# Kernel optimization log

Measured on AMD Instinct MI355X. Metric: run time of the kernel, lower is better.

Reference implementation:

```python
import jax, jax.numpy as jnp
import numpy as np

N_NODES = 50000
NEG_SLOPE = 0.2  # PyG GATConv default leaky-relu slope


def _gat_conv(x, edge_index, W, a_src, a_dst, bias, heads, out_ch, concat, num_nodes):
    # x: [N, F_in]; W: [F_in, heads*out_ch]; a_src/a_dst: [heads, out_ch]; bias: [heads*out_ch] or [out_ch]
    h = (x @ W).reshape(num_nodes, heads, out_ch)            # [N,H,C]
    alpha_src = jnp.einsum('nhc,hc->nh', h, a_src)           # [N,H]
    alpha_dst = jnp.einsum('nhc,hc->nh', h, a_dst)           # [N,H]
    src, dst = edge_index[0], edge_index[1]
    e = jax.nn.leaky_relu(alpha_src[src] + alpha_dst[dst], NEG_SLOPE)  # [E,H]
    # segment softmax over incoming edges per destination (self-loops guarantee non-empty segments)
    m = jax.ops.segment_max(e, dst, num_segments=num_nodes)
    e = jnp.exp(e - m[dst])
    denom = jax.ops.segment_sum(e, dst, num_segments=num_nodes)
    alpha = e / denom[dst]                                    # [E,H]
    msg = h[src] * alpha[:, :, None]                          # [E,H,C]
    out = jax.ops.segment_sum(msg, dst, num_segments=num_nodes)  # [N,H,C]
    if concat:
        out = out.reshape(num_nodes, heads * out_ch)
    else:
        out = out.mean(axis=1)
    return out + bias


def _add_self_loops(edge_index, num_nodes):
    loops = jnp.arange(num_nodes, dtype=edge_index.dtype)
    return jnp.concatenate([edge_index, jnp.stack([loops, loops])], axis=1)


def setup_inputs() -> dict:
    key = jax.random.key(0)
    ks = jax.random.split(key, 16)
    N, F_in, H, C_hid, C_out = N_NODES, 128, 4, 64, 64
    E = 800000
    x = jax.random.normal(ks[0], (N, F_in), dtype=jnp.float32)
    edge_index = jax.random.randint(ks[1], (2, E), 0, N, dtype=jnp.int32)
    s = lambda fan: 1.0 / np.sqrt(fan)
    inp = {
        'x': x, 'edge_index': edge_index,
        'W1': jax.random.normal(ks[2], (F_in, H * C_hid), jnp.float32) * s(F_in),
        'a_src1': jax.random.normal(ks[3], (H, C_hid), jnp.float32) * s(C_hid),
        'a_dst1': jax.random.normal(ks[4], (H, C_hid), jnp.float32) * s(C_hid),
        'b1': jnp.zeros((H * C_hid,), jnp.float32),
        'W2': jax.random.normal(ks[5], (H * C_hid, H * C_hid), jnp.float32) * s(H * C_hid),
        'a_src2': jax.random.normal(ks[6], (H, C_hid), jnp.float32) * s(C_hid),
        'a_dst2': jax.random.normal(ks[7], (H, C_hid), jnp.float32) * s(C_hid),
        'b2': jnp.zeros((H * C_hid,), jnp.float32),
        'W3': jax.random.normal(ks[8], (H * C_hid, C_out), jnp.float32) * s(H * C_hid),
        'a_src3': jax.random.normal(ks[9], (1, C_out), jnp.float32) * s(C_out),
        'a_dst3': jax.random.normal(ks[10], (1, C_out), jnp.float32) * s(C_out),
        'b3': jnp.zeros((C_out,), jnp.float32),
    }
    return inp


def reference(x, edge_index, W1, a_src1, a_dst1, b1, W2, a_src2, a_dst2, b2, W3, a_src3, a_dst3, b3):
    N = x.shape[0]
    ei = _add_self_loops(edge_index, N)
    h = _gat_conv(x, ei, W1, a_src1, a_dst1, b1, heads=4, out_ch=64, concat=True, num_nodes=N)
    h = jax.nn.elu(h)
    h = _gat_conv(h, ei, W2, a_src2, a_dst2, b2, heads=4, out_ch=64, concat=True, num_nodes=N)
    h = jax.nn.elu(h)
    out = _gat_conv(h, ei, W3, a_src3, a_dst3, b3, heads=1, out_ch=64, concat=False, num_nodes=N)
    return out
```

## Files before the change

### kernel.cpp

```cpp
#include <hip/hip_runtime.h>
#include <hip/hip_fp16.h>
#include <cstdint>


typedef _Float16 f16;
typedef _Float16 f16x8 __attribute__((ext_vector_type(8)));
typedef float f32x4 __attribute__((ext_vector_type(4)));

__global__ __launch_bounds__(256) void count_kernel(const int* __restrict__ ei,
                                                    int E, int N,
                                                    int* __restrict__ deg) {
  int g = blockIdx.x * 256 + threadIdx.x;
  if (g >= E + N) return;
  int dst = (g < E) ? ei[E + g] : (g - E);
  atomicAdd(&deg[dst], 1);
}

__global__ __launch_bounds__(256) void deg_block_reduce(const int* __restrict__ deg,
                                                        int* __restrict__ bsum, int N) {
  __shared__ int red[4];
  int b = blockIdx.x;
  int v = 0;
#pragma unroll
  for (int s = 0; s < 4; ++s) {
    int idx = b * 1024 + s * 256 + threadIdx.x;
    if (idx < N) v += deg[idx];
  }
  for (int off = 32; off; off >>= 1) v += __shfl_down(v, off);
  if ((threadIdx.x & 63) == 0) red[threadIdx.x >> 6] = v;
  __syncthreads();
  if (threadIdx.x == 0) bsum[b] = red[0] + red[1] + red[2] + red[3];
}

__global__ __launch_bounds__(1024) void small_scan(const int* __restrict__ bsum,
                                                   int* __restrict__ bpre, int NB) {
  __shared__ int buf[1024];
  int v = (threadIdx.x < NB) ? bsum[threadIdx.x] : 0;
  buf[threadIdx.x] = v;
  __syncthreads();
  for (int off = 1; off < 1024; off <<= 1) {
    int tv = (threadIdx.x >= off) ? buf[threadIdx.x - off] : 0;
    __syncthreads();
    buf[threadIdx.x] += tv;
    __syncthreads();
  }
  if (threadIdx.x < NB) bpre[threadIdx.x] = buf[threadIdx.x] - v;
}

__global__ __launch_bounds__(1024) void scan_final(const int* __restrict__ deg,
                                                   const int* __restrict__ bpre,
                                                   int* __restrict__ row_off,
                                                   int* __restrict__ cursor,
                                                   int N, int total) {
  __shared__ int buf[1024];
  int b = blockIdx.x;
  int i = b * 1024 + threadIdx.x;
  int v = (i < N) ? deg[i] : 0;
  buf[threadIdx.x] = v;
  __syncthreads();
  for (int off = 1; off < 1024; off <<= 1) {
    int tv = (threadIdx.x >= off) ? buf[threadIdx.x - off] : 0;
    __syncthreads();
    buf[threadIdx.x] += tv;
    __syncthreads();
  }
  if (i < N) {
    int ro = bpre[b] + buf[threadIdx.x] - v;
    row_off[i] = ro;
    cursor[i] = ro;
  }
  if (i == 0) row_off[N] = total;
}

__global__ __launch_bounds__(256) void scatter_kernel(const int* __restrict__ ei,
                                                      int E, int N,
                                                      int* __restrict__ cursor,
                                                      int* __restrict__ esrc,
                                                      int* __restrict__ edst) {
  int g = blockIdx.x * 256 + threadIdx.x;
  if (g >= E + N) return;
  int src, dst;
  if (g < E) { src = ei[g]; dst = ei[E + g]; }
  else       { src = g - E; dst = src; }
  int pos = atomicAdd(&cursor[dst], 1);
  esrc[pos] = src;
  edst[pos] = dst;
}

__global__ __launch_bounds__(256) void convert_wt_all(
    const float* __restrict__ W1, const float* __restrict__ W2,
    const float* __restrict__ W3, f16* __restrict__ Wt1, f16* __restrict__ Wt2,
    f16* __restrict__ Wt3, int n1, int n2, int n3, int N1, int N2, int N3,
    int K1, int K2, int K3) {
  int t = blockIdx.x * 256 + threadIdx.x;
  if (t < n1) {
    int n = t % N1, k = t / N1;
    Wt1[(size_t)n * K1 + k] = (f16)W1[t];
    return;
  }
  t -= n1;
  if (t < n2) {
    int n = t % N2, k = t / N2;
    Wt2[(size_t)n * K2 + k] = (f16)W2[t];
    return;
  }
  t -= n2;
  if (t < n3) {
    int n = t % N3, k = t / N3;
    Wt3[(size_t)n * K3 + k] = (f16)W3[t];
  }
}

template <int BN, bool ACAST>
__global__ __launch_bounds__(256) void mfma_gemm_alpha(
    const void* __restrict__ Ap_, const f16* __restrict__ Bt,
    f16* __restrict__ Tout,
    const float* __restrict__ avec_src, const float* __restrict__ avec_dst,
    float* __restrict__ asrc, float* __restrict__ adst,
    int M, int K, int Ncol) {
  constexpr int RF = (BN == 128) ? 4 : 2;
  __shared__ f16 As[128][40];
  __shared__ f16 Bs[BN][40];
  int tid = threadIdx.x;
  int wv = tid >> 6, lane = tid & 63;
  int lrow = lane & 15, lkb = lane >> 4;
  int row0 = blockIdx.x * 128, col0 = blockIdx.y * BN;
  int wro = (BN == 128) ? (wv >> 1) * 64 : wv * 32;
  int wco = (BN == 128) ? (wv & 1) * 64 : 0;
  int hg = (col0 + wco) >> 6;

  f32x4 acc[RF][4];
#pragma unroll
  for (int rf = 0; rf < RF; ++rf)
#pragma unroll
    for (int cf = 0; cf < 4; ++cf) acc[rf][cf] = (f32x4){0.f, 0.f, 0.f, 0.f};

  for (int kk = 0; kk < K; kk += 32) {
#pragma unroll
    for (int q = 0; q < 2; ++q) {
      int slot = tid + q * 256;
      int r = slot >> 2, ko = (slot & 3) << 3;
      int gr = min(row0 + r, M - 1);
      if (ACAST) {
        const float* Af = (const float*)Ap_ + (size_t)gr * K + kk + ko;
        float4 v0 = *reinterpret_cast<const float4*>(Af);
        float4 v1 = *reinterpret_cast<const float4*>(Af + 4);
        f16 o[8] = {(f16)v0.x, (f16)v0.y, (f16)v0.z, (f16)v0.w,
                    (f16)v1.x, (f16)v1.y, (f16)v1.z, (f16)v1.w};
        *reinterpret_cast<f16x8*>(&As[r][ko]) = *reinterpret_cast<f16x8*>(o);
      } else {
        *reinterpret_cast<f16x8*>(&As[r][ko]) =
            *reinterpret_cast<const f16x8*>((const f16*)Ap_ + (size_t)gr * K + kk + ko);
      }
    }
#pragma unroll
    for (int q = 0; q < BN / 64; ++q) {
      int slot = tid + q * 256;
      int c = slot >> 2, ko = (slot & 3) << 3;
      *reinterpret_cast<f16x8*>(&Bs[c][ko]) =
          *reinterpret_cast<const f16x8*>(&Bt[(size_t)(col0 + c) * K + kk + ko]);
    }
    __syncthreads();
    f16x8 af[RF], bf[4];
#pragma unroll
    for (int rf = 0; rf < RF; ++rf)
      af[rf] = *reinterpret_cast<f16x8*>(&As[wro + rf * 16 + lrow][lkb * 8]);
#pragma unroll
    for (int cf = 0; cf < 4; ++cf)
      bf[cf] = *reinterpret_cast<f16x8*>(&Bs[wco + cf * 16 + lrow][lkb * 8]);
#pragma unroll
    for (int rf = 0; rf < RF; ++rf)
#pragma unroll
      for (int cf = 0; cf < 4; ++cf)
        acc[rf][cf] = __builtin_amdgcn_mfma_f32_16x16x32_f16(af[rf], bf[cf],
                                                             acc[rf][cf], 0, 0, 0);
    __syncthreads();
  }

  int Hh = Ncol >> 6;
  float avs[4], avd[4];
#pragma unroll
  for (int cf = 0; cf < 4; ++cf) {
    avs[cf] = avec_src[hg * 64 + cf * 16 + lrow];
    avd[cf] = avec_dst[hg * 64 + cf * 16 + lrow];
  }

#pragma unroll
  for (int rf = 0; rf < RF; ++rf) {
#pragma unroll
    for (int r = 0; r < 4; ++r) {
      float ps = 0.f, pd = 0.f;
#pragma unroll
      for (int cf = 0; cf < 4; ++cf) {
        float v = acc[rf][cf][r];
        ps = fmaf(v, avs[cf], ps);
        pd = fmaf(v, avd[cf], pd);
      }
#pragma unroll
      for (int off = 1; off < 16; off <<= 1) {
        ps += __shfl_xor(ps, off);
        pd += __shfl_xor(pd, off);
      }
      int row = row0 + wro + rf * 16 + lkb * 4 + r;
      if (lrow == 0 && row < M) {
        asrc[row * Hh + hg] = ps;
        adst[row * Hh + hg] = pd;
      }
    }
#pragma unroll
    for (int r = 0; r < 4; ++r) {
      int row = row0 + wro + rf * 16 + lkb * 4 + r;
      if (row < M) {
#pragma unroll
        for (int cf = 0; cf < 4; ++cf)
          Tout[(size_t)row * Ncol + col0 + wco + cf * 16 + lrow] =
              (f16)acc[rf][cf][r];
      }
    }
  }
}

__global__ __launch_bounds__(256) void edge_weights_h4(
    const int* __restrict__ esrc, const int* __restrict__ edst,
    const float* __restrict__ asrc, const float* __restrict__ adst,
    float* __restrict__ w, int ET) {
  int t = blockIdx.x * 256 + threadIdx.x;
  if (t >= ET * 4) return;
  int j = t >> 2, h = t & 3;
  float e = asrc[esrc[j] * 4 + h] + adst[edst[j] * 4 + h];
  e = fmaxf(e, 0.2f * e);
  w[t] = __expf(e);
}

__global__ __launch_bounds__(256) void edge_weights_h1(
    const int* __restrict__ esrc, const int* __restrict__ edst,
    const float* __restrict__ asrc, const float* __restrict__ adst,
    float* __restrict__ w, int ET) {
  int j = blockIdx.x * 256 + threadIdx.x;
  if (j >= ET) return;
  float e = asrc[esrc[j]] + adst[edst[j]];
  e = fmaxf(e, 0.2f * e);
  w[j] = __expf(e);
}

template <bool ELU>
__global__ __launch_bounds__(256) void aggregate_h4(
    const f16* __restrict__ T16, const int* __restrict__ row_off,
    const int* __restrict__ esrc, const float* __restrict__ w,
    const float* __restrict__ bias, f16* __restrict__ outF, int N) {
  int wv = threadIdx.x >> 6, lane = threadIdx.x & 63;
  int dst = blockIdx.x * 4 + wv;
  if (dst >= N) return;
  int head = lane >> 4;
  int hsel = lane & 48;
  int r0 = row_off[dst], r1 = row_off[dst + 1];
  const char* tbase = reinterpret_cast<const char*>(T16);
  uint loff = (uint)lane * 8;
  float den = 0.f, ax = 0.f, ay = 0.f, az = 0.f, aw = 0.f;
  for (int base = r0; base < r1; base += 8) {
    int jb = base + (lane & 7);
    int sv = 0;
    float wl = 0.f;
    if (jb < r1) {
      sv = esrc[jb];
      wl = w[(jb << 2) + head];
    }
#pragma unroll
    for (int i = 0; i < 8; ++i) {
      int sj = __shfl(sv, i);
      float wj = __shfl(wl, hsel + i);
      den += wj;
      uint2 raw = *reinterpret_cast<const uint2*>(tbase + (((uint)sj << 9) + loff));
      __half2 p0 = *reinterpret_cast<__half2*>(&raw.x);
      __half2 p1 = *reinterpret_cast<__half2*>(&raw.y);
      float2 f0 = __half22float2(p0);
      float2 f1 = __half22float2(p1);
      ax = fmaf(wj, f0.x, ax);
      ay = fmaf(wj, f0.y, ay);
      az = fmaf(wj, f1.x, az);
      aw = fmaf(wj, f1.y, aw);
    }
  }
  float rd = 1.f / den;
  float4 bv = *reinterpret_cast<const float4*>(&bias[lane << 2]);
  float vx = ax * rd + bv.x, vy = ay * rd + bv.y;
  float vz = az * rd + bv.z, vw = aw * rd + bv.w;
  if (ELU) {
    vx = vx > 0.f ? vx : expm1f(vx);
    vy = vy > 0.f ? vy : expm1f(vy);
    vz = vz > 0.f ? vz : expm1f(vz);
    vw = vw > 0.f ? vw : expm1f(vw);
  }
  f16 o[4] = {(f16)vx, (f16)vy, (f16)vz, (f16)vw};
  *reinterpret_cast<uint2*>(&outF[(size_t)dst * 256 + (lane << 2)]) =
      *reinterpret_cast<uint2*>(o);
}

__global__ __launch_bounds__(256) void aggregate_h1(
    const f16* __restrict__ T16, const int* __restrict__ row_off,
    const int* __restrict__ esrc, const float* __restrict__ w,
    const float* __restrict__ bias, float* __restrict__ out, int N) {
  int wv = threadIdx.x >> 6, lane = threadIdx.x & 63;
  int grp = lane >> 4, l = lane & 15;
  int gsel = lane & 48;
  int dst = blockIdx.x * 16 + wv * 4 + grp;
  if (dst >= N) return;
  int r0 = row_off[dst], r1 = row_off[dst + 1];
  const char* tbase = reinterpret_cast<const char*>(T16);
  uint loff = (uint)l * 8;
  float den = 0.f, ax = 0.f, ay = 0.f, az = 0.f, aw = 0.f;
  for (int base = r0; base < r1; base += 8) {
    int jb = base + (l & 7);
    int sv = 0;
    float wl = 0.f;
    if (jb < r1) {
      sv = esrc[jb];
      wl = w[jb];
    }
#pragma unroll
    for (int i = 0; i < 8; ++i) {
      int sj = __shfl(sv, gsel + i);
      float wj = __shfl(wl, gsel + i);
      den += wj;
      uint2 raw = *reinterpret_cast<const uint2*>(tbase + (((uint)sj << 7) + loff));
      __half2 p0 = *reinterpret_cast<__half2*>(&raw.x);
      __half2 p1 = *reinterpret_cast<__half2*>(&raw.y);
      float2 f0 = __half22float2(p0);
      float2 f1 = __half22float2(p1);
      ax = fmaf(wj, f0.x, ax);
      ay = fmaf(wj, f0.y, ay);
      az = fmaf(wj, f1.x, az);
      aw = fmaf(wj, f1.y, aw);
    }
  }
  float rd = 1.f / den;
  float4 v;
  v.x = ax * rd + bias[l * 4 + 0];
  v.y = ay * rd + bias[l * 4 + 1];
  v.z = az * rd + bias[l * 4 + 2];
  v.w = aw * rd + bias[l * 4 + 3];
  *reinterpret_cast<float4*>(&out[(size_t)dst * 64 + l * 4]) = v;
}

extern "C" void kernel_launch(void* const* d_in, const int* in_sizes, int n_in,
                              void* d_out, int out_size, void* d_ws, size_t ws_size,
                              hipStream_t stream) {
  const float* x   = (const float*)d_in[0];
  const int*   ei  = (const int*)d_in[1];
  const float* W1  = (const float*)d_in[2];
  const float* as1 = (const float*)d_in[3];
  const float* ad1 = (const float*)d_in[4];
  const float* b1  = (const float*)d_in[5];
  const float* W2  = (const float*)d_in[6];
  const float* as2 = (const float*)d_in[7];
  const float* ad2 = (const float*)d_in[8];
  const float* b2  = (const float*)d_in[9];
  const float* W3  = (const float*)d_in[10];
  const float* as3 = (const float*)d_in[11];
  const float* ad3 = (const float*)d_in[12];
  const float* b3  = (const float*)d_in[13];
  float* out = (float*)d_out;

  const int Fin = 128, H = 4, C = 64, HC = H * C;
  const int N = in_sizes[0] / Fin;
  const int E = in_sizes[1] / 2;
  const int ET = E + N;
  const int NB = (N + 1023) / 1024;

  f16* T16   = (f16*)d_ws;
  f16* F16   = T16 + (size_t)N * HC;
  f16* T16L3 = F16 + (size_t)N * HC;
  f16* Wt1   = T16L3 + (size_t)N * C;
  f16* Wt2   = Wt1 + HC * Fin;
  f16* Wt3   = Wt2 + HC * HC;
  float* asrc = (float*)(Wt3 + C * HC);
  float* adst = asrc + (size_t)N * H;
  float* wbuf = adst + (size_t)N * H;
  int* deg     = (int*)(wbuf + (size_t)ET * 4);
  int* row_off = deg + N;
  int* cursor  = row_off + (N + 1);
  int* bsum    = cursor + N;
  int* bpre    = bsum + NB;
  int* esrc    = bpre + NB;
  int* edst    = esrc + ET;

  hipMemsetAsync(deg, 0, N * sizeof(int), stream);
  count_kernel<<<(ET + 255) / 256, 256, 0, stream>>>(ei, E, N, deg);
  deg_block_reduce<<<NB, 256, 0, stream>>>(deg, bsum, N);
  small_scan<<<1, 1024, 0, stream>>>(bsum, bpre, NB);
  scan_final<<<NB, 1024, 0, stream>>>(deg, bpre, row_off, cursor, N, ET);
  scatter_kernel<<<(ET + 255) / 256, 256, 0, stream>>>(ei, E, N, cursor, esrc, edst);

  int n1 = Fin * HC, n2 = HC * HC, n3 = HC * C;
  convert_wt_all<<<(n1 + n2 + n3 + 255) / 256, 256, 0, stream>>>(
      W1, W2, W3, Wt1, Wt2, Wt3, n1, n2, n3, HC, HC, C, Fin, HC, HC);

  int gx = (N + 127) / 128;
  int eb4 = (ET * 4 + 255) / 256, eb1 = (ET + 255) / 256;
  int ab4 = (N + 3) / 4;
  int ab1 = (N + 15) / 16;

  mfma_gemm_alpha<128, true><<<dim3(gx, 2), 256, 0, stream>>>(
      x, Wt1, T16, as1, ad1, asrc, adst, N, Fin, HC);
  edge_weights_h4<<<eb4, 256, 0, stream>>>(esrc, edst, asrc, adst, wbuf, ET);
  aggregate_h4<true><<<ab4, 256, 0, stream>>>(T16, row_off, esrc, wbuf, b1, F16, N);

  mfma_gemm_alpha<128, false><<<dim3(gx, 2), 256, 0, stream>>>(
      F16, Wt2, T16, as2, ad2, asrc, adst, N, HC, HC);
  edge_weights_h4<<<eb4, 256, 0, stream>>>(esrc, edst, asrc, adst, wbuf, ET);
  aggregate_h4<true><<<ab4, 256, 0, stream>>>(T16, row_off, esrc, wbuf, b2, F16, N);

  mfma_gemm_alpha<64, false><<<dim3(gx, 1), 256, 0, stream>>>(
      F16, Wt3, T16L3, as3, ad3, asrc, adst, N, HC, C);
  edge_weights_h1<<<eb1, 256, 0, stream>>>(esrc, edst, asrc, adst, wbuf, ET);
  aggregate_h1<<<ab1, 256, 0, stream>>>(T16L3, row_off, esrc, wbuf, b3, out, N);
}
```

Baseline: 325.7 us.

## Permute feature layout so GEMM epilogue stores vectorized, pre-convert x to fp16

```diff
diff --git a/kernel.cpp b/kernel.cpp
--- a/kernel.cpp
+++ b/kernel.cpp
@@ -87,33 +87,42 @@
   edst[pos] = dst;
 }
 
-__global__ __launch_bounds__(256) void convert_wt_all(
-    const float* __restrict__ W1, const float* __restrict__ W2,
-    const float* __restrict__ W3, f16* __restrict__ Wt1, f16* __restrict__ Wt2,
-    f16* __restrict__ Wt3, int n1, int n2, int n3, int N1, int N2, int N3,
-    int K1, int K2, int K3) {
+__global__ __launch_bounds__(256) void convert_all(
+    const float* __restrict__ x, const float* __restrict__ W1,
+    const float* __restrict__ W2, const float* __restrict__ W3,
+    f16* __restrict__ xh, f16* __restrict__ Wt1, f16* __restrict__ Wt2,
+    f16* __restrict__ Wt3, int nx4, int n1, int n2, int n3) {
   int t = blockIdx.x * 256 + threadIdx.x;
+  if (t < nx4) {
+    float4 v = *reinterpret_cast<const float4*>(&x[t * 4]);
+    f16 o[4] = {(f16)v.x, (f16)v.y, (f16)v.z, (f16)v.w};
+    *reinterpret_cast<uint2*>(&xh[t * 4]) = *reinterpret_cast<uint2*>(o);
+    return;
+  }
+  t -= nx4;
   if (t < n1) {
-    int n = t % N1, k = t / N1;
-    Wt1[(size_t)n * K1 + k] = (f16)W1[t];
+    int n = t % 256, k = t / 256;
+    Wt1[(size_t)n * 128 + k] = (f16)W1[t];
     return;
   }
   t -= n1;
   if (t < n2) {
-    int n = t % N2, k = t / N2;
-    Wt2[(size_t)n * K2 + k] = (f16)W2[t];
+    int n = t % 256, k = t / 256;
+    int kp = (k & 192) | ((k & 15) << 2) | ((k >> 4) & 3);
+    Wt2[(size_t)n * 256 + kp] = (f16)W2[t];
     return;
   }
   t -= n2;
   if (t < n3) {
-    int n = t % N3, k = t / N3;
-    Wt3[(size_t)n * K3 + k] = (f16)W3[t];
-  }
-}
-
-template <int BN, bool ACAST>
+    int n = t % 64, k = t / 64;
+    int kp = (k & 192) | ((k & 15) << 2) | ((k >> 4) & 3);
+    Wt3[(size_t)n * 256 + kp] = (f16)W3[t];
+  }
+}
+
+template <int BN>
 __global__ __launch_bounds__(256) void mfma_gemm_alpha(
-    const void* __restrict__ Ap_, const f16* __restrict__ Bt,
+    const f16* __restrict__ A, const f16* __restrict__ Bt,
     f16* __restrict__ Tout,
     const float* __restrict__ avec_src, const float* __restrict__ avec_dst,
     float* __restrict__ asrc, float* __restrict__ adst,
@@ -141,17 +150,8 @@
       int slot = tid + q * 256;
       int r = slot >> 2, ko = (slot & 3) << 3;
       int gr = min(row0 + r, M - 1);
-      if (ACAST) {
-        const float* Af = (const float*)Ap_ + (size_t)gr * K + kk + ko;
-        float4 v0 = *reinterpret_cast<const float4*>(Af);
-        float4 v1 = *reinterpret_cast<const float4*>(Af + 4);
-        f16 o[8] = {(f16)v0.x, (f16)v0.y, (f16)v0.z, (f16)v0.w,
-                    (f16)v1.x, (f16)v1.y, (f16)v1.z, (f16)v1.w};
-        *reinterpret_cast<f16x8*>(&As[r][ko]) = *reinterpret_cast<f16x8*>(o);
-      } else {
-        *reinterpret_cast<f16x8*>(&As[r][ko]) =
-            *reinterpret_cast<const f16x8*>((const f16*)Ap_ + (size_t)gr * K + kk + ko);
-      }
+      *reinterpret_cast<f16x8*>(&As[r][ko]) =
+          *reinterpret_cast<const f16x8*>(&A[(size_t)gr * K + kk + ko]);
     }
 #pragma unroll
     for (int q = 0; q < BN / 64; ++q) {
@@ -211,10 +211,11 @@
     for (int r = 0; r < 4; ++r) {
       int row = row0 + wro + rf * 16 + lkb * 4 + r;
       if (row < M) {
-#pragma unroll
-        for (int cf = 0; cf < 4; ++cf)
-          Tout[(size_t)row * Ncol + col0 + wco + cf * 16 + lrow] =
-              (f16)acc[rf][cf][r];
+        f16 o[4] = {(f16)acc[rf][0][r], (f16)acc[rf][1][r],
+                    (f16)acc[rf][2][r], (f16)acc[rf][3][r]};
+        *reinterpret_cast<uint2*>(
+            &Tout[(size_t)row * Ncol + col0 + wco + (lrow << 2)]) =
+            *reinterpret_cast<uint2*>(o);
       }
     }
   }
@@ -282,9 +283,12 @@
     }
   }
   float rd = 1.f / den;
-  float4 bv = *reinterpret_cast<const float4*>(&bias[lane << 2]);
-  float vx = ax * rd + bv.x, vy = ay * rd + bv.y;
-  float vz = az * rd + bv.z, vw = aw * rd + bv.w;
+  int l = lane & 15;
+  int bb = hsel * 4 + l;
+  float vx = ax * rd + bias[bb];
+  float vy = ay * rd + bias[bb + 16];
+  float vz = az * rd + bias[bb + 32];
+  float vw = aw * rd + bias[bb + 48];
   if (ELU) {
     vx = vx > 0.f ? vx : expm1f(vx);
     vy = vy > 0.f ? vy : expm1f(vy);
@@ -334,12 +338,10 @@
     }
   }
   float rd = 1.f / den;
-  float4 v;
-  v.x = ax * rd + bias[l * 4 + 0];
-  v.y = ay * rd + bias[l * 4 + 1];
-  v.z = az * rd + bias[l * 4 + 2];
-  v.w = aw * rd + bias[l * 4 + 3];
-  *reinterpret_cast<float4*>(&out[(size_t)dst * 64 + l * 4]) = v;
+  out[(size_t)dst * 64 + l]      = ax * rd + bias[l];
+  out[(size_t)dst * 64 + 16 + l] = ay * rd + bias[16 + l];
+  out[(size_t)dst * 64 + 32 + l] = az * rd + bias[32 + l];
+  out[(size_t)dst * 64 + 48 + l] = aw * rd + bias[48 + l];
 }
 
 extern "C" void kernel_launch(void* const* d_in, const int* in_sizes, int n_in,
@@ -367,7 +369,8 @@
   const int ET = E + N;
   const int NB = (N + 1023) / 1024;
 
-  f16* T16   = (f16*)d_ws;
+  f16* xh    = (f16*)d_ws;
+  f16* T16   = xh + (size_t)N * Fin;
   f16* F16   = T16 + (size_t)N * HC;
   f16* T16L3 = F16 + (size_t)N * HC;
   f16* Wt1   = T16L3 + (size_t)N * C;
@@ -391,26 +394,27 @@
   scan_final<<<NB, 1024, 0, stream>>>(deg, bpre, row_off, cursor, N, ET);
   scatter_kernel<<<(ET + 255) / 256, 256, 0, stream>>>(ei, E, N, cursor, esrc, edst);
 
+  int nx4 = N * Fin / 4;
   int n1 = Fin * HC, n2 = HC * HC, n3 = HC * C;
-  convert_wt_all<<<(n1 + n2 + n3 + 255) / 256, 256, 0, stream>>>(
-      W1, W2, W3, Wt1, Wt2, Wt3, n1, n2, n3, HC, HC, C, Fin, HC, HC);
+  convert_all<<<(nx4 + n1 + n2 + n3 + 255) / 256, 256, 0, stream>>>(
+      x, W1, W2, W3, xh, Wt1, Wt2, Wt3, nx4, n1, n2, n3);
 
   int gx = (N + 127) / 128;
   int eb4 = (ET * 4 + 255) / 256, eb1 = (ET + 255) / 256;
   int ab4 = (N + 3) / 4;
   int ab1 = (N + 15) / 16;
 
-  mfma_gemm_alpha<128, true><<<dim3(gx, 2), 256, 0, stream>>>(
-      x, Wt1, T16, as1, ad1, asrc, adst, N, Fin, HC);
+  mfma_gemm_alpha<128><<<dim3(gx, 2), 256, 0, stream>>>(
+      xh, Wt1, T16, as1, ad1, asrc, adst, N, Fin, HC);
   edge_weights_h4<<<eb4, 256, 0, stream>>>(esrc, edst, asrc, adst, wbuf, ET);
   aggregate_h4<true><<<ab4, 256, 0, stream>>>(T16, row_off, esrc, wbuf, b1, F16, N);
 
-  mfma_gemm_alpha<128, false><<<dim3(gx, 2), 256, 0, stream>>>(
+  mfma_gemm_alpha<128><<<dim3(gx, 2), 256, 0, stream>>>(
       F16, Wt2, T16, as2, ad2, asrc, adst, N, HC, HC);
   edge_weights_h4<<<eb4, 256, 0, stream>>>(esrc, edst, asrc, adst, wbuf, ET);
   aggregate_h4<true><<<ab4, 256, 0, stream>>>(T16, row_off, esrc, wbuf, b2, F16, N);
 
-  mfma_gemm_alpha<64, false><<<dim3(gx, 1), 256, 0, stream>>>(
+  mfma_gemm_alpha<64><<<dim3(gx, 1), 256, 0, stream>>>(
       F16, Wt3, T16L3, as3, ad3, asrc, adst, N, HC, C);
   edge_weights_h1<<<eb1, 256, 0, stream>>>(esrc, edst, asrc, adst, wbuf, ET);
   aggregate_h1<<<ab1, 256, 0, stream>>>(T16L3, row_off, esrc, wbuf, b3, out, N);
```

After: 328.7 us. Within noise of the previous version (+0.9%).
